# Performance work log

Hardware: AMD Instinct MI355X
Metric: run time of the kernel (lower is better)

Reference implementation:

```python
import jax, jax.numpy as jnp
import numpy as np

N_SLICES, H, W = 64, 64, 64
VD, VH, VW = 64, 64, 64
K = 3            # PSF kernel size per axis
RES = 1.5        # res_s / res_r
GAP = 1.0        # through-plane slice spacing in recon voxels
N_ITER = 2       # CG iterations (init kwarg)


def _rotmat(ax, ay, az):
    cx, sx = np.cos(ax), np.sin(ax)
    cy, sy = np.cos(ay), np.sin(ay)
    cz, sz = np.cos(az), np.sin(az)
    Rx = np.array([[1, 0, 0], [0, cx, -sx], [0, sx, cx]])
    Ry = np.array([[cy, 0, sy], [0, 1, 0], [-sy, 0, cy]])
    Rz = np.array([[cz, -sz, 0], [sz, cz, 0], [0, 0, 1]])
    return Rz @ Ry @ Rx


def setup_inputs() -> dict:
    rng = np.random.default_rng(0)
    R = np.stack([_rotmat(*rng.normal(0.0, 0.05, 3)) for _ in range(N_SLICES)])
    t = np.zeros((N_SLICES, 3))
    t[:, :2] = rng.normal(0.0, 1.0, (N_SLICES, 2))
    t[:, 2] = (np.arange(N_SLICES) - (N_SLICES - 1) / 2) * GAP + rng.normal(0.0, 0.3, N_SLICES)
    transforms = jnp.asarray(np.concatenate([R, t[:, :, None]], -1), jnp.float32)  # (S,3,4)
    k1, k2 = jax.random.split(jax.random.key(0))
    slices = jax.random.uniform(k1, (N_SLICES, H, W), jnp.float32)
    volume = jax.random.uniform(k2, (VD, VH, VW), jnp.float32) * 0.1
    g = np.arange(K) - (K - 1) / 2
    gz, gy, gx = np.meshgrid(g, g, g, indexing='ij')
    psf = np.exp(-(gx ** 2 + gy ** 2) / (2 * 0.6 ** 2) - gz ** 2 / (2 * 1.0 ** 2))
    psf = jnp.asarray(psf / psf.sum(), jnp.float32)
    return {"transforms": transforms, "slices": slices, "volume": volume, "psf": psf}


def _positions(transforms):
    # PSF sample positions of every slice pixel, mapped into volume voxel coords (xyz).
    xs = (jnp.arange(W) - (W - 1) / 2) * RES
    ys = (jnp.arange(H) - (H - 1) / 2) * RES
    o = jnp.arange(K) - (K - 1) / 2
    oz, oy, ox = jnp.meshgrid(o, o, o, indexing='ij')
    off = jnp.stack([ox, oy, oz], -1).reshape(-1, 3)              # (K^3, 3)
    base = jnp.stack(jnp.broadcast_arrays(xs[None, :], ys[:, None], jnp.zeros((H, W))), -1)
    pts = base[None] + off[:, None, None, :]                      # (K^3, H, W, 3) slice frame
    R, tr = transforms[:, :, :3], transforms[:, :, 3]
    pos = jnp.einsum('sij,khwj->skhwi', R, pts) + tr[:, None, None, None, :]
    center = jnp.array([(VW - 1) / 2, (VH - 1) / 2, (VD - 1) / 2], jnp.float32)
    return pos + center                                           # (S, K^3, H, W, 3)


def _corner_iter(pos):
    # yields the 8 trilinear corners: (clipped int indices (z,y,x), weight with OOB zeroed)
    x, y, z = pos[..., 0], pos[..., 1], pos[..., 2]
    x0, y0, z0 = jnp.floor(x), jnp.floor(y), jnp.floor(z)
    fx, fy, fz = x - x0, y - y0, z - z0
    for dz in (0, 1):
        for dy in (0, 1):
            for dx in (0, 1):
                xi, yi, zi = x0 + dx, y0 + dy, z0 + dz
                w = (fx if dx else 1 - fx) * (fy if dy else 1 - fy) * (fz if dz else 1 - fz)
                valid = (xi >= 0) & (xi < VW) & (yi >= 0) & (yi < VH) & (zi >= 0) & (zi < VD)
                w = jnp.where(valid, w, 0.0)
                yield (jnp.clip(zi, 0, VD - 1).astype(jnp.int32),
                       jnp.clip(yi, 0, VH - 1).astype(jnp.int32),
                       jnp.clip(xi, 0, VW - 1).astype(jnp.int32)), w


def _A(vol, pos, psf_flat):
    # slice_acquisition: trilinear gather + PSF-weighted sum -> (S,H,W)
    acc = jnp.zeros(pos.shape[:-1], vol.dtype)
    for (zi, yi, xi), w in _corner_iter(pos):
        acc = acc + w * vol[zi, yi, xi]
    return jnp.einsum('k,skhw->shw', psf_flat, acc)


def _At(slc, pos, psf_flat):
    # slice_acquisition_adjoint: PSF-weighted trilinear scatter-add -> (VD,VH,VW)
    vals = psf_flat[None, :, None, None] * slc[:, None]           # (S,K^3,H,W)
    vol = jnp.zeros((VD, VH, VW), slc.dtype)
    for (zi, yi, xi), w in _corner_iter(pos):
        vol = vol.at[zi, yi, xi].add(w * vals)
    return vol


def _cg(Afun, b, x0, n_iter):
    x = x0
    r = b - Afun(x)
    p = r
    rr = jnp.vdot(r, r)
    for i in range(n_iter):
        Ap = Afun(p)
        alpha = rr / jnp.vdot(p, Ap)
        x = x + alpha * p
        if i == n_iter - 1:
            break
        r = r - alpha * Ap
        rr_new = jnp.vdot(r, r)
        p = r + (rr_new / rr) * p
        rr = rr_new
    return x


def reference(transforms, slices, volume, psf):
    pos = _positions(transforms)
    psf_flat = psf.reshape(-1)
    AtA = lambda v: _At(_A(v, pos, psf_flat), pos, psf_flat)
    b = _At(slices, pos, psf_flat)
    x = _cg(AtA, b, volume, N_ITER)
    return jax.nn.relu(x)
```

## Files before the change

kernel.cpp:

```cpp
#include <hip/hip_runtime.h>

#define NS 64
#define HH 64
#define WW 64
#define VD 64
#define VH 64
#define VW 64
#define NVOX (VD*VH*VW)
#define NPIX (NS*HH*WW)
#define RES 1.5f
#define NTAB (NS*27)
#define WIN 6
#define SPLIT 8
#define COL_PAD 67

__global__ __launch_bounds__(256) void k_setup(const float* __restrict__ tr,
                                               const float* __restrict__ psf,
                                               float* __restrict__ tab) {
    int i = blockIdx.x * 256 + threadIdx.x;
    if (i >= NTAB) return;
    int s = i / 27, k = i % 27;
    const float* p = tr + s * 12;
    float R00 = p[0], R01 = p[1], R02 = p[2],  t0 = p[3];
    float R10 = p[4], R11 = p[5], R12 = p[6],  t1 = p[7];
    float R20 = p[8], R21 = p[9], R22 = p[10], t2 = p[11];
    float Ux = RES * R00, Uy = RES * R10, Uz = RES * R20;
    float Vx = RES * R01, Vy = RES * R11, Vz = RES * R21;
    float ox = (float)(k % 3 - 1), oy = (float)((k / 3) % 3 - 1), oz = (float)(k / 9 - 1);
    float Cx = t0 + 31.5f + R00 * ox + R01 * oy + R02 * oz - 31.5f * (Ux + Vx);
    float Cy = t1 + 31.5f + R10 * ox + R11 * oy + R12 * oz - 31.5f * (Uy + Vy);
    float Cz = t2 + 31.5f + R20 * ox + R21 * oy + R22 * oz - 31.5f * (Uz + Vz);
    float inv = 1.f / (Ux * Vy - Uy * Vx);
    float* e = tab + i * 16;
    e[0] = Vy * inv;  e[1] = -Vx * inv; e[2] = -Uy * inv; e[3] = Ux * inv;
    e[4] = Ux; e[5] = Uy; e[6] = Uz; e[7] = Vx;
    e[8] = Vy; e[9] = Vz; e[10] = Cx; e[11] = Cy;
    e[12] = Cz; e[13] = psf[k]; e[14] = 0.f; e[15] = 0.f;
}

__device__ __forceinline__ float trilin_gather_bf(const float* __restrict__ vol,
                                                  float px, float py, float pz) {
    float x0 = floorf(px), y0 = floorf(py), z0 = floorf(pz);
    float fx = px - x0, fy = py - y0, fz = pz - z0;
    int ix = (int)x0, iy = (int)y0, iz = (int)z0;

    float wx0 = ((unsigned)ix       < 64u) ? (1.f - fx) : 0.f;
    float wx1 = ((unsigned)(ix + 1) < 64u) ? fx         : 0.f;
    float wy0 = ((unsigned)iy       < 64u) ? (1.f - fy) : 0.f;
    float wy1 = ((unsigned)(iy + 1) < 64u) ? fy         : 0.f;
    float wz0 = ((unsigned)iz       < 64u) ? (1.f - fz) : 0.f;
    float wz1 = ((unsigned)(iz + 1) < 64u) ? fz         : 0.f;

    int xc0 = min(max(ix, 0), 63),     xc1 = min(max(ix + 1, 0), 63);
    int yc0 = min(max(iy, 0), 63) << 6,  yc1 = min(max(iy + 1, 0), 63) << 6;
    int zc0 = min(max(iz, 0), 63) << 12, zc1 = min(max(iz + 1, 0), 63) << 12;

    float v000 = vol[zc0 + yc0 + xc0], v001 = vol[zc0 + yc0 + xc1];
    float v010 = vol[zc0 + yc1 + xc0], v011 = vol[zc0 + yc1 + xc1];
    float v100 = vol[zc1 + yc0 + xc0], v101 = vol[zc1 + yc0 + xc1];
    float v110 = vol[zc1 + yc1 + xc0], v111 = vol[zc1 + yc1 + xc1];

    float w00 = wx0 * wy0, w01 = wx1 * wy0, w10 = wx0 * wy1, w11 = wx1 * wy1;
    float lo = fmaf(w00, v000, fmaf(w01, v001, fmaf(w10, v010, w11 * v011)));
    float hi = fmaf(w00, v100, fmaf(w01, v101, fmaf(w10, v110, w11 * v111)));
    return fmaf(wz0, lo, wz1 * hi);
}

template<bool SUB>
__global__ __launch_bounds__(256) void k_a(const float* __restrict__ vin,
                                           float* __restrict__ g,
                                           const float* __restrict__ tr,
                                           const float* __restrict__ psf,
                                           const float* __restrict__ slc) {
    __shared__ float s_psf[27];
    if (threadIdx.x < 27) s_psf[threadIdx.x] = psf[threadIdx.x];
    __syncthreads();
    int gid = blockIdx.x * 256 + threadIdx.x;
    int pixel = gid >> 2, q = gid & 3;
    int s = pixel >> 12;
    int pix = pixel & 4095;
    int h = pix >> 6, w = pix & 63;
    const float* p = tr + s * 12;
    float R0 = p[0], R1 = p[1], R2 = p[2],  t0 = p[3];
    float R3 = p[4], R4 = p[5], R5 = p[6],  t1 = p[7];
    float R6 = p[8], R7 = p[9], R8 = p[10], t2 = p[11];
    float xs = ((float)w - 31.5f) * RES;
    float ys = ((float)h - 31.5f) * RES;
    float p0x = fmaf(R0, xs, fmaf(R1, ys, t0)) + 31.5f;
    float p0y = fmaf(R3, xs, fmaf(R4, ys, t1)) + 31.5f;
    float p0z = fmaf(R6, xs, fmaf(R7, ys, t2)) + 31.5f;
    float a = 0.f;
#pragma unroll
    for (int j = 0; j < 7; ++j) {
        int k = q + 4 * j;
        if (k < 27) {
            float ox = (float)(k % 3 - 1), oy = (float)((k / 3) % 3 - 1), oz = (float)(k / 9 - 1);
            float px = p0x + ox * R0 + oy * R1 + oz * R2;
            float py = p0y + ox * R3 + oy * R4 + oz * R5;
            float pz = p0z + ox * R6 + oy * R7 + oz * R8;
            a = fmaf(s_psf[k], trilin_gather_bf(vin, px, py, pz), a);
        }
    }
    a += __shfl_xor(a, 1);
    a += __shfl_xor(a, 2);
    if (q == 0) g[pixel] = SUB ? (slc[pixel] - a) : a;
}

__device__ __forceinline__ void block_reduce_atomic(float v, float* dst) {
#pragma unroll
    for (int off = 32; off > 0; off >>= 1) v += __shfl_down(v, off, 64);
    __shared__ float s_red[4];
    int lane = threadIdx.x & 63, wid = threadIdx.x >> 6;
    if (lane == 0) s_red[wid] = v;
    __syncthreads();
    if (threadIdx.x == 0) atomicAdd(dst, s_red[0] + s_red[1] + s_red[2] + s_red[3]);
}

__global__ __launch_bounds__(512, 8) void k_atv(const float* __restrict__ g,
                                                float* __restrict__ part,
                                                const float* __restrict__ tab) {
    __shared__ float stab[8 * 27 * 16];
    __shared__ float cols[32][COL_PAD];

    int tid = threadIdx.x;
    int Yb    = blockIdx.x >> 4;
    int xhalf = (blockIdx.x >> 3) & 1;
    int split = blockIdx.x & 7;

    {
        const float4* src = (const float4*)(tab + split * 8 * 27 * 16);
        float4* dst = (float4*)stab;
#pragma unroll
        for (int i = 0; i < 2; ++i) {
            int j = tid + i * 512;
            if (j < 864) dst[j] = src[j];
        }
    }
    {
        float4* c4 = (float4*)&cols[0][0];
#pragma unroll
        for (int i = 0; i < 2; ++i) {
            int j = tid + i * 512;
            if (j < 536) c4[j] = make_float4(0.f, 0.f, 0.f, 0.f);
        }
    }
    __syncthreads();

    int xl   = tid & 31;
    int half = (tid >> 5) & 1;
    int sg   = tid >> 6;
    int s    = split * 8 + sg;
    float X = (float)(xhalf * 32 + xl);
    float Y = (float)Yb;

    const float* tb = stab + sg * 27 * 16;
    int gbase = s << 12;

    const float* ec = tb + 13 * 16;
    float4 c0 = *(const float4*)(ec);
    float4 c1 = *(const float4*)(ec + 4);
    float4 c2 = *(const float4*)(ec + 8);
    float4 c3 = *(const float4*)(ec + 12);
    float rxc = X - c2.z, ryc = Y - c2.w;
    float wsc = c0.x * rxc + c0.y * ryc;
    float hsc = c0.z * rxc + c0.w * ryc;
    float pzc = fmaf(wsc, c1.z, fmaf(hsc, c2.y, c3.x));
    float basef = floorf(pzc) - 2.f;
    int   basei = (int)basef;

    float acc[WIN];
#pragma unroll
    for (int j = 0; j < WIN; ++j) acc[j] = 0.f;

    int kbeg = half * 14;
    int kend = kbeg + 14 - half;
    for (int k = kbeg; k < kend; ++k) {
        const float* e = tb + k * 16;
        float4 e0 = *(const float4*)(e);
        float4 e1 = *(const float4*)(e + 4);
        float4 e2 = *(const float4*)(e + 8);
        float4 e3 = *(const float4*)(e + 12);
        float Ux = e1.x, Uy = e1.y, Uz = e1.z, Vx = e1.w;
        float Vy = e2.x, Vz = e2.y;
        float Cxr = e2.z - X, Cyr = e2.w - Y;
        float psfk = e3.y;
        float ws = e0.x * (-Cxr) + e0.y * (-Cyr);
        float hs = e0.z * (-Cxr) + e0.w * (-Cyr);
        float w0f = floorf(ws), h0f = floorf(hs);
        int w0 = (int)w0f, h0 = (int)h0f;
#pragma unroll
        for (int dh = 0; dh < 2; ++dh) {
            float fh = h0f + (float)dh;
            int hi = h0 + dh;
            int hok = ((unsigned)hi < 64u) ? 1 : 0;
            int hc = min(max(hi, 0), 63);
            float tx = fmaf(fh, Vx, Cxr);
            float ty = fmaf(fh, Vy, Cyr);
            float tz = fmaf(fh, Vz, e3.x);
#pragma unroll
            for (int dw = 0; dw < 2; ++dw) {
                float fw = w0f + (float)dw;
                int wi = w0 + dw;
                int ok = ((unsigned)wi < 64u) ? hok : 0;
                int wc = min(max(wi, 0), 63);
                float ddx = fmaf(fw, Ux, tx);
                float ddy = fmaf(fw, Uy, ty);
                float wx = fmaxf(0.f, 1.f - fabsf(ddx));
                float wy = fmaxf(0.f, 1.f - fabsf(ddy));
                float gv = g[gbase + (hc << 6) + wc];
                float val = ok ? (wx * wy * psfk * gv) : 0.f;
                float prel = fmaf(fw, Uz, tz) - basef;
#pragma unroll
                for (int j = 0; j < WIN; ++j) {
                    float t = fmaxf(0.f, 1.f - fabsf(prel - (float)j));
                    acc[j] = fmaf(val, t, acc[j]);
                }
            }
        }
    }

#pragma unroll
    for (int j = 0; j < WIN; ++j) {
        int zj = basei + j;
        int okz = ((unsigned)zj < 64u);
        int zc = min(max(zj, 0), 63);
        atomicAdd(&cols[xl][zc], okz ? acc[j] : 0.f);
    }
    __syncthreads();

    float* pout = part + split * NVOX + (Yb << 6) + xhalf * 32;
#pragma unroll
    for (int i = 0; i < 4; ++i) {
        int j = tid + i * 512;
        int z = j >> 5, x = j & 31;
        pout[(z << 12) + x] = cols[x][z];
    }
}


__device__ __forceinline__ float sum8(const float* __restrict__ part, int i) {
    float a = 0.f;
#pragma unroll
    for (int j = 0; j < SPLIT; ++j) a += part[j * NVOX + i];
    return a;
}

__global__ __launch_bounds__(256) void k_residual8(const float* __restrict__ part,
                                                   float* __restrict__ r,
                                                   float* __restrict__ p,
                                                   float* __restrict__ scal) {
    int i = blockIdx.x * 256 + threadIdx.x;
    float rv = sum8(part, i);
    r[i] = rv;
    p[i] = rv;
    block_reduce_atomic(rv * rv, &scal[0]);
}

__global__ __launch_bounds__(256) void k_dot_reduce8(const float* __restrict__ part,
                                                     const float* __restrict__ p,
                                                     float* __restrict__ Ap,
                                                     float* __restrict__ dst) {
    int i = blockIdx.x * 256 + threadIdx.x;
    float apv = sum8(part, i);
    Ap[i] = apv;
    block_reduce_atomic(p[i] * apv, dst);
}

__global__ __launch_bounds__(256) void k_dot8(const float* __restrict__ part,
                                              const float* __restrict__ p,
                                              float* __restrict__ dst) {
    int i = blockIdx.x * 256 + threadIdx.x;
    block_reduce_atomic(p[i] * sum8(part, i), dst);
}

__global__ __launch_bounds__(256) void k_update_xr(const float* __restrict__ x_in,
                                                   float* __restrict__ x_out,
                                                   float* __restrict__ r,
                                                   const float* __restrict__ p,
                                                   const float* __restrict__ Ap,
                                                   float* __restrict__ scal) {
    int i = blockIdx.x * 256 + threadIdx.x;
    float alpha = scal[0] / scal[1];
    x_out[i] = fmaf(alpha, p[i], x_in[i]);
    float rv = fmaf(-alpha, Ap[i], r[i]);
    r[i] = rv;
    block_reduce_atomic(rv * rv, &scal[2]);
}

__global__ __launch_bounds__(256) void k_update_p(float* __restrict__ p,
                                                  const float* __restrict__ r,
                                                  const float* __restrict__ scal) {
    int i = blockIdx.x * 256 + threadIdx.x;
    float beta = scal[2] / scal[0];
    p[i] = fmaf(beta, p[i], r[i]);
}

__global__ __launch_bounds__(256) void k_final(const float* __restrict__ x,
                                               const float* __restrict__ p,
                                               const float* __restrict__ scal,
                                               float* __restrict__ out) {
    int i = blockIdx.x * 256 + threadIdx.x;
    float alpha = scal[2] / scal[3];
    float v = fmaf(alpha, p[i], x[i]);
    out[i] = v > 0.f ? v : 0.f;
}

extern "C" void kernel_launch(void* const* d_in, const int* in_sizes, int n_in,
                              void* d_out, int out_size, void* d_ws, size_t ws_size,
                              hipStream_t stream) {
    const float* transforms = (const float*)d_in[0];
    const float* slices     = (const float*)d_in[1];
    const float* volume     = (const float*)d_in[2];
    const float* psf        = (const float*)d_in[3];
    float* out = (float*)d_out;

    float* tab    = (float*)d_ws;
    float* part   = tab    + NTAB * 16;
    float* vol_x  = part   + SPLIT * NVOX;
    float* vol_r  = vol_x  + NVOX;
    float* vol_p  = vol_r  + NVOX;
    float* gbuf   = vol_p  + NVOX;
    float* scal   = gbuf   + NPIX;
    float* Ap     = gbuf;

    const int ablk = 64 * 2 * SPLIT;
    const int fblk = NPIX * 4 / 256;
    const int vblk = NVOX / 256;

    hipMemsetAsync(scal, 0, 4 * sizeof(float), stream);

    k_setup<<<(NTAB + 255) / 256, 256, 0, stream>>>(transforms, psf, tab);

    k_a<true><<<fblk, 256, 0, stream>>>(volume, gbuf, transforms, psf, slices);
    k_atv<<<ablk, 512, 0, stream>>>(gbuf, part, tab);
    k_residual8<<<vblk, 256, 0, stream>>>(part, vol_r, vol_p, scal);

    k_a<false><<<fblk, 256, 0, stream>>>(vol_p, gbuf, transforms, psf, nullptr);
    k_atv<<<ablk, 512, 0, stream>>>(gbuf, part, tab);
    k_dot_reduce8<<<vblk, 256, 0, stream>>>(part, vol_p, Ap, &scal[1]);
    k_update_xr<<<vblk, 256, 0, stream>>>(volume, vol_x, vol_r, vol_p, Ap, scal);
    k_update_p<<<vblk, 256, 0, stream>>>(vol_p, vol_r, scal);

    k_a<false><<<fblk, 256, 0, stream>>>(vol_p, gbuf, transforms, psf, nullptr);
    k_atv<<<ablk, 512, 0, stream>>>(gbuf, part, tab);
    k_dot8<<<vblk, 256, 0, stream>>>(part, vol_p, &scal[3]);
    k_final<<<vblk, 256, 0, stream>>>(vol_x, vol_p, scal, out);
}
```

Baseline: 298.0 us.

## Pad slice residual buffer, halve split count, and pack z-window accumulation into float2

The slice-space residual is now stored in a zero-padded 66x68 per-slice layout, so the adjoint gather no longer needs per-tap bounds checks and clamps. Each thread handles all 27 PSF taps for one slice (16 slices per block, SPLIT 4), which halves the partial-volume buffers and the reduction reads. The 6-tap z hat-weight accumulation uses 2-wide float vectors to allow packed FMA/min/max. The risks are lower occupancy from the doubled shared table and launch bounds of (512,4), fewer blocks, and an extra memset of the padded buffer.

```diff
diff --git a/kernel.cpp b/kernel.cpp
--- a/kernel.cpp
+++ b/kernel.cpp
@@ -1,4 +1,6 @@
 #include <hip/hip_runtime.h>
+
+typedef __attribute__((ext_vector_type(2))) float f32x2;
 
 #define NS 64
 #define HH 64
@@ -11,8 +13,11 @@
 #define RES 1.5f
 #define NTAB (NS*27)
 #define WIN 6
-#define SPLIT 8
+#define SPLIT 4
 #define COL_PAD 67
+#define GP_ROW 68
+#define GP_SLC (66*GP_ROW)
+#define GP_TOT (NS*GP_SLC)
 
 __global__ __launch_bounds__(256) void k_setup(const float* __restrict__ tr,
                                                const float* __restrict__ psf,
@@ -32,9 +37,9 @@
     float Cz = t2 + 31.5f + R20 * ox + R21 * oy + R22 * oz - 31.5f * (Uz + Vz);
     float inv = 1.f / (Ux * Vy - Uy * Vx);
     float* e = tab + i * 16;
-    e[0] = Vy * inv;  e[1] = -Vx * inv; e[2] = -Uy * inv; e[3] = Ux * inv;
-    e[4] = Ux; e[5] = Uy; e[6] = Uz; e[7] = Vx;
-    e[8] = Vy; e[9] = Vz; e[10] = Cx; e[11] = Cy;
+    e[0] = Vy * inv;  e[1] = -Uy * inv;  e[2] = -Vx * inv; e[3] = Ux * inv;
+    e[4] = Ux; e[5] = Uy; e[6] = Vx; e[7] = Vy;
+    e[8] = Uz; e[9] = Vz; e[10] = Cx; e[11] = Cy;
     e[12] = Cz; e[13] = psf[k]; e[14] = 0.f; e[15] = 0.f;
 }
 
@@ -68,7 +73,7 @@
 
 template<bool SUB>
 __global__ __launch_bounds__(256) void k_a(const float* __restrict__ vin,
-                                           float* __restrict__ g,
+                                           float* __restrict__ gp,
                                            const float* __restrict__ tr,
                                            const float* __restrict__ psf,
                                            const float* __restrict__ slc) {
@@ -103,7 +108,7 @@
     }
     a += __shfl_xor(a, 1);
     a += __shfl_xor(a, 2);
-    if (q == 0) g[pixel] = SUB ? (slc[pixel] - a) : a;
+    if (q == 0) gp[s * GP_SLC + (h + 1) * GP_ROW + (w + 1)] = SUB ? (slc[pixel] - a) : a;
 }
 
 __device__ __forceinline__ void block_reduce_atomic(float v, float* dst) {
@@ -116,24 +121,24 @@
     if (threadIdx.x == 0) atomicAdd(dst, s_red[0] + s_red[1] + s_red[2] + s_red[3]);
 }
 
-__global__ __launch_bounds__(512, 8) void k_atv(const float* __restrict__ g,
+__global__ __launch_bounds__(512, 4) void k_atv(const float* __restrict__ g,
                                                 float* __restrict__ part,
                                                 const float* __restrict__ tab) {
-    __shared__ float stab[8 * 27 * 16];
+    __shared__ float stab[16 * 27 * 16];
     __shared__ float cols[32][COL_PAD];
 
     int tid = threadIdx.x;
-    int Yb    = blockIdx.x >> 4;
-    int xhalf = (blockIdx.x >> 3) & 1;
-    int split = blockIdx.x & 7;
+    int Yb    = blockIdx.x >> 3;
+    int xhalf = (blockIdx.x >> 2) & 1;
+    int split = blockIdx.x & 3;
 
     {
-        const float4* src = (const float4*)(tab + split * 8 * 27 * 16);
+        const float4* src = (const float4*)(tab + split * 16 * 27 * 16);
         float4* dst = (float4*)stab;
 #pragma unroll
-        for (int i = 0; i < 2; ++i) {
+        for (int i = 0; i < 4; ++i) {
             int j = tid + i * 512;
-            if (j < 864) dst[j] = src[j];
+            if (j < 1728) dst[j] = src[j];
         }
     }
     {
@@ -146,85 +151,89 @@
     }
     __syncthreads();
 
-    int xl   = tid & 31;
-    int half = (tid >> 5) & 1;
-    int sg   = tid >> 6;
-    int s    = split * 8 + sg;
+    int xl = tid & 31;
+    int sg = tid >> 5;
+    int s  = split * 16 + sg;
     float X = (float)(xhalf * 32 + xl);
     float Y = (float)Yb;
 
     const float* tb = stab + sg * 27 * 16;
-    int gbase = s << 12;
-
+    int gbase = s * GP_SLC;
+
+    {
+    }
     const float* ec = tb + 13 * 16;
-    float4 c0 = *(const float4*)(ec);
-    float4 c1 = *(const float4*)(ec + 4);
-    float4 c2 = *(const float4*)(ec + 8);
-    float4 c3 = *(const float4*)(ec + 12);
-    float rxc = X - c2.z, ryc = Y - c2.w;
-    float wsc = c0.x * rxc + c0.y * ryc;
-    float hsc = c0.z * rxc + c0.w * ryc;
-    float pzc = fmaf(wsc, c1.z, fmaf(hsc, c2.y, c3.x));
+    float4 ce0 = *(const float4*)(ec);
+    float4 ce2 = *(const float4*)(ec + 8);
+    float4 ce3 = *(const float4*)(ec + 12);
+    float rxc = X - ce2.z, ryc = Y - ce2.w;
+    float wsc = ce0.x * rxc + ce0.z * ryc;
+    float hsc = ce0.y * rxc + ce0.w * ryc;
+    float pzc = fmaf(wsc, ce2.x, fmaf(hsc, ce2.y, ce3.x));
     float basef = floorf(pzc) - 2.f;
     int   basei = (int)basef;
 
-    float acc[WIN];
-#pragma unroll
-    for (int j = 0; j < WIN; ++j) acc[j] = 0.f;
-
-    int kbeg = half * 14;
-    int kend = kbeg + 14 - half;
-    for (int k = kbeg; k < kend; ++k) {
+    f32x2 a01 = {0.f, 0.f}, a23 = {0.f, 0.f}, a45 = {0.f, 0.f};
+    const f32x2 zero2 = {0.f, 0.f};
+    const f32x2 cA0 = {1.f, 2.f}, cB0 = {-1.f, 0.f};
+    const f32x2 cA1 = {3.f, 4.f}, cB1 = {1.f, 2.f};
+    const f32x2 cA2 = {5.f, 6.f}, cB2 = {3.f, 4.f};
+
+#pragma unroll 3
+    for (int k = 0; k < 27; ++k) {
         const float* e = tb + k * 16;
         float4 e0 = *(const float4*)(e);
         float4 e1 = *(const float4*)(e + 4);
         float4 e2 = *(const float4*)(e + 8);
         float4 e3 = *(const float4*)(e + 12);
-        float Ux = e1.x, Uy = e1.y, Uz = e1.z, Vx = e1.w;
-        float Vy = e2.x, Vz = e2.y;
-        float Cxr = e2.z - X, Cyr = e2.w - Y;
+        float rx = X - e2.z, ry = Y - e2.w;
+        float ws = e0.x * rx + e0.z * ry;
+        float hs = e0.y * rx + e0.w * ry;
+        float w0f = __builtin_amdgcn_fmed3f(floorf(ws), -1.f, 63.f);
+        float h0f = __builtin_amdgcn_fmed3f(floorf(hs), -1.f, 63.f);
+        int wA = (int)w0f, hA = (int)h0f;
+        float Ux = e1.x, Uy = e1.y, Vx = e1.z, Vy = e1.w;
+        float Uz = e2.x, Vz = e2.y;
+        float Czb = e3.x - basef;
         float psfk = e3.y;
-        float ws = e0.x * (-Cxr) + e0.y * (-Cyr);
-        float hs = e0.z * (-Cxr) + e0.w * (-Cyr);
-        float w0f = floorf(ws), h0f = floorf(hs);
-        int w0 = (int)w0f, h0 = (int)h0f;
+        float Cxr = -rx, Cyr = -ry;
+        int colbase = gbase + wA + 1;
 #pragma unroll
         for (int dh = 0; dh < 2; ++dh) {
             float fh = h0f + (float)dh;
-            int hi = h0 + dh;
-            int hok = ((unsigned)hi < 64u) ? 1 : 0;
-            int hc = min(max(hi, 0), 63);
-            float tx = fmaf(fh, Vx, Cxr);
-            float ty = fmaf(fh, Vy, Cyr);
-            float tz = fmaf(fh, Vz, e3.x);
+            float tx  = fmaf(fh, Vx, Cxr);
+            float ty  = fmaf(fh, Vy, Cyr);
+            float tzb = fmaf(fh, Vz, Czb);
+            int rowoff = colbase + (hA + 1 + dh) * GP_ROW;
 #pragma unroll
             for (int dw = 0; dw < 2; ++dw) {
                 float fw = w0f + (float)dw;
-                int wi = w0 + dw;
-                int ok = ((unsigned)wi < 64u) ? hok : 0;
-                int wc = min(max(wi, 0), 63);
                 float ddx = fmaf(fw, Ux, tx);
                 float ddy = fmaf(fw, Uy, ty);
-                float wx = fmaxf(0.f, 1.f - fabsf(ddx));
-                float wy = fmaxf(0.f, 1.f - fabsf(ddy));
-                float gv = g[gbase + (hc << 6) + wc];
-                float val = ok ? (wx * wy * psfk * gv) : 0.f;
-                float prel = fmaf(fw, Uz, tz) - basef;
-#pragma unroll
-                for (int j = 0; j < WIN; ++j) {
-                    float t = fmaxf(0.f, 1.f - fabsf(prel - (float)j));
-                    acc[j] = fmaf(val, t, acc[j]);
-                }
+                float wx = fmaxf(1.f - fabsf(ddx), 0.f);
+                float wy = fmaxf(1.f - fabsf(ddy), 0.f);
+                float gv = g[rowoff + dw];
+                float val = wx * wy * psfk * gv;
+                float prel = fmaf(fw, Uz, tzb);
+                f32x2 v2 = {val, val};
+                f32x2 p2 = {prel, prel};
+                a01 += v2 * __builtin_elementwise_max(zero2,
+                          __builtin_elementwise_min(cA0 - p2, p2 - cB0));
+                a23 += v2 * __builtin_elementwise_max(zero2,
+                          __builtin_elementwise_min(cA1 - p2, p2 - cB1));
+                a45 += v2 * __builtin_elementwise_max(zero2,
+                          __builtin_elementwise_min(cA2 - p2, p2 - cB2));
             }
         }
     }
 
+    float accs[WIN] = {a01.x, a01.y, a23.x, a23.y, a45.x, a45.y};
 #pragma unroll
     for (int j = 0; j < WIN; ++j) {
         int zj = basei + j;
         int okz = ((unsigned)zj < 64u);
         int zc = min(max(zj, 0), 63);
-        atomicAdd(&cols[xl][zc], okz ? acc[j] : 0.f);
+        atomicAdd(&cols[xl][zc], okz ? accs[j] : 0.f);
     }
     __syncthreads();
 
@@ -238,39 +247,36 @@
 }
 
 
-__device__ __forceinline__ float sum8(const float* __restrict__ part, int i) {
-    float a = 0.f;
-#pragma unroll
-    for (int j = 0; j < SPLIT; ++j) a += part[j * NVOX + i];
-    return a;
-}
-
-__global__ __launch_bounds__(256) void k_residual8(const float* __restrict__ part,
+__device__ __forceinline__ float sum4p(const float* __restrict__ part, int i) {
+    return (part[i] + part[NVOX + i]) + (part[2 * NVOX + i] + part[3 * NVOX + i]);
+}
+
+__global__ __launch_bounds__(256) void k_residual4(const float* __restrict__ part,
                                                    float* __restrict__ r,
                                                    float* __restrict__ p,
                                                    float* __restrict__ scal) {
     int i = blockIdx.x * 256 + threadIdx.x;
-    float rv = sum8(part, i);
+    float rv = sum4p(part, i);
     r[i] = rv;
     p[i] = rv;
     block_reduce_atomic(rv * rv, &scal[0]);
 }
 
-__global__ __launch_bounds__(256) void k_dot_reduce8(const float* __restrict__ part,
+__global__ __launch_bounds__(256) void k_dot_reduce4(const float* __restrict__ part,
                                                      const float* __restrict__ p,
                                                      float* __restrict__ Ap,
                                                      float* __restrict__ dst) {
     int i = blockIdx.x * 256 + threadIdx.x;
-    float apv = sum8(part, i);
+    float apv = sum4p(part, i);
     Ap[i] = apv;
     block_reduce_atomic(p[i] * apv, dst);
 }
 
-__global__ __launch_bounds__(256) void k_dot8(const float* __restrict__ part,
+__global__ __launch_bounds__(256) void k_dot4(const float* __restrict__ part,
                                               const float* __restrict__ p,
                                               float* __restrict__ dst) {
     int i = blockIdx.x * 256 + threadIdx.x;
-    block_reduce_atomic(p[i] * sum8(part, i), dst);
+    block_reduce_atomic(p[i] * sum4p(part, i), dst);
 }
 
 __global__ __launch_bounds__(256) void k_update_xr(const float* __restrict__ x_in,
@@ -315,34 +321,34 @@
     float* out = (float*)d_out;
 
     float* tab    = (float*)d_ws;
-    float* part   = tab    + NTAB * 16;
+    float* gbuf   = tab    + NTAB * 16;
+    float* scal   = gbuf   + GP_TOT;
+    float* part   = scal   + 8;
     float* vol_x  = part   + SPLIT * NVOX;
     float* vol_r  = vol_x  + NVOX;
     float* vol_p  = vol_r  + NVOX;
-    float* gbuf   = vol_p  + NVOX;
-    float* scal   = gbuf   + NPIX;
-    float* Ap     = gbuf;
+    float* Ap     = vol_p  + NVOX;
 
     const int ablk = 64 * 2 * SPLIT;
     const int fblk = NPIX * 4 / 256;
     const int vblk = NVOX / 256;
 
-    hipMemsetAsync(scal, 0, 4 * sizeof(float), stream);
+    hipMemsetAsync(gbuf, 0, (GP_TOT + 8) * sizeof(float), stream);
 
     k_setup<<<(NTAB + 255) / 256, 256, 0, stream>>>(transforms, psf, tab);
 
     k_a<true><<<fblk, 256, 0, stream>>>(volume, gbuf, transforms, psf, slices);
     k_atv<<<ablk, 512, 0, stream>>>(gbuf, part, tab);
-    k_residual8<<<vblk, 256, 0, stream>>>(part, vol_r, vol_p, scal);
+    k_residual4<<<vblk, 256, 0, stream>>>(part, vol_r, vol_p, scal);
 
     k_a<false><<<fblk, 256, 0, stream>>>(vol_p, gbuf, transforms, psf, nullptr);
     k_atv<<<ablk, 512, 0, stream>>>(gbuf, part, tab);
-    k_dot_reduce8<<<vblk, 256, 0, stream>>>(part, vol_p, Ap, &scal[1]);
+    k_dot_reduce4<<<vblk, 256, 0, stream>>>(part, vol_p, Ap, &scal[1]);
     k_update_xr<<<vblk, 256, 0, stream>>>(volume, vol_x, vol_r, vol_p, Ap, scal);
     k_update_p<<<vblk, 256, 0, stream>>>(vol_p, vol_r, scal);
 
     k_a<false><<<fblk, 256, 0, stream>>>(vol_p, gbuf, transforms, psf, nullptr);
     k_atv<<<ablk, 512, 0, stream>>>(gbuf, part, tab);
-    k_dot8<<<vblk, 256, 0, stream>>>(part, vol_p, &scal[3]);
+    k_dot4<<<vblk, 256, 0, stream>>>(part, vol_p, &scal[3]);
     k_final<<<vblk, 256, 0, stream>>>(vol_x, vol_p, scal, out);
 }
```

New measurement: 289.9 us. -2.7%, faster.
